# Optimization experiments

Hardware: AMD Instinct MI355X
Metric: run time of the kernel (lower is better)

Reference implementation:

```python
import jax, jax.numpy as jnp
import numpy as np

B, IN_DIM, OUT_DIM, N_KNOTS = 8192, 1024, 1024, 4


def setup_inputs() -> dict:
    key = jax.random.key(0)
    k_feat, k_phase, k_w = jax.random.split(key, 3)
    feats = jax.random.normal(k_feat, (B, IN_DIM), dtype=jnp.float32)
    phase = jax.random.uniform(k_phase, (B, 1), dtype=jnp.float32)  # phase in [0,1)
    x = jnp.concatenate([feats, phase], axis=1)  # [B, IN_DIM+1]
    bound = np.sqrt(6.0 / (OUT_DIM * IN_DIM))
    weight_knots = jax.random.uniform(
        k_w, (N_KNOTS, OUT_DIM, IN_DIM), dtype=jnp.float32, minval=-bound, maxval=bound)
    bias_knots = jnp.zeros((N_KNOTS, OUT_DIM), dtype=jnp.float32)
    return {"x": x, "weight_knots": weight_knots, "bias_knots": bias_knots}


def _cubic(y, mu):
    # Catmull-Rom cubic blend over the 4 gathered knots, y: [B,4,D], mu: [B,1]
    y0, y1, y2, y3 = y[:, 0], y[:, 1], y[:, 2], y[:, 3]
    return ((-0.5 * y0 + 1.5 * y1 - 1.5 * y2 + 0.5 * y3) * mu * mu * mu
            + (y0 - 2.5 * y1 + 2.0 * y2 - 0.5 * y3) * mu * mu
            + (-0.5 * y0 + 0.5 * y2) * mu + y1)


def reference(x, weight_knots, bias_knots):
    K = weight_knots.shape[0]
    phase = x[:, -1]            # [B]
    feats = x[:, :-1]           # [B, IN_DIM]
    pscale = K * phase
    mu = jnp.mod(pscale, 1.0)[:, None]                       # [B, 1]
    i1 = jnp.mod(pscale.astype(jnp.int32), K)
    idx = jnp.stack([jnp.mod(i1 - 1, K), i1,
                     jnp.mod(i1 + 1, K), jnp.mod(i1 + 2, K)], axis=1)  # [B, 4]
    # Exploit linearity: matvec against each knot matrix once, then blend.
    # Mathematically identical to cubic(W0,..,W3) @ feats + cubic(b0,..,b3).
    yk = jnp.einsum('koi,bi->bko', weight_knots, feats)      # [B, K, OUT]
    y4 = jnp.take_along_axis(yk, idx[:, :, None], axis=1)    # [B, 4, OUT]
    b4 = bias_knots[idx]                                     # [B, 4, OUT]
    res = _cubic(y4 + b4, mu)                                # cubic is linear in y
    return jax.nn.elu(res)
```

## Files before the change

kernel.cpp:

```cpp
#include <hip/hip_runtime.h>
#include <math.h>

#define IN_DIM 1024
#define OUT_DIM 1024
#define NROWS 8192
#define XSTRIDE 1025

typedef __attribute__((ext_vector_type(8))) short bf16x8;
typedef __attribute__((ext_vector_type(4))) float f32x4;

static __device__ __forceinline__ unsigned f2bf(float f) {
  union { float f; unsigned u; } v; v.f = f;
  unsigned u = v.u;
  return (u + 0x7fffu + ((u >> 16) & 1u)) >> 16;
}

__global__ __launch_bounds__(256) void prep_kernel(
    const float* __restrict__ x, const float* __restrict__ W,
    unsigned short* __restrict__ Wb, unsigned short* __restrict__ F,
    float* __restrict__ coef)
{
  const int blk = blockIdx.x;
  if (blk < 2048) {
    const int t = blk * 256 + threadIdx.x;
    const int flat = t * 8;
    const int k = flat >> 20;
    const int o = (flat >> 10) & 1023;
    const int i = flat & 1023;
    const float4 fa = *reinterpret_cast<const float4*>(W + flat);
    const float4 fb = *reinterpret_cast<const float4*>(W + flat + 4);
    uint4 pk;
    pk.x = f2bf(fa.x) | (f2bf(fa.y) << 16);
    pk.y = f2bf(fa.z) | (f2bf(fa.w) << 16);
    pk.z = f2bf(fb.x) | (f2bf(fb.y) << 16);
    pk.w = f2bf(fb.z) | (f2bf(fb.w) << 16);
    const int g = (o & 15) | (k << 4) | ((o >> 4) << 6);
    *reinterpret_cast<uint4*>(Wb + (size_t)g * 1024 + i) = pk;
  } else {
    const int b = blk - 2048;
    const float* xr = x + (size_t)b * XSTRIDE;
    const int i = threadIdx.x * 4;
    ushort4 vv;
    vv.x = (unsigned short)f2bf(xr[i]);     vv.y = (unsigned short)f2bf(xr[i + 1]);
    vv.z = (unsigned short)f2bf(xr[i + 2]); vv.w = (unsigned short)f2bf(xr[i + 3]);
    *reinterpret_cast<ushort4*>(F + (size_t)b * 1024 + i) = vv;
    if (threadIdx.x == 0) {
      const float ps = 4.0f * xr[IN_DIM];
      const int ip = (int)ps;
      const int i1 = ip & 3;
      const float mu = ps - (float)ip;
      const float mu2 = mu * mu, mu3 = mu2 * mu;
      const float c0 = -0.5f * mu3 +        mu2 - 0.5f * mu;
      const float c1 =  1.5f * mu3 - 2.5f * mu2 + 1.0f;
      const float c2 = -1.5f * mu3 + 2.0f * mu2 + 0.5f * mu;
      const float c3 =  0.5f * mu3 - 0.5f * mu2;
      const int d0 = (0-i1)&3, d1 = (1-i1)&3, d2 = (2-i1)&3, d3 = (3-i1)&3;
      float4 cv;
      cv.x = d0==0 ? c1 : d0==1 ? c2 : d0==2 ? c3 : c0;
      cv.y = d1==0 ? c1 : d1==1 ? c2 : d1==2 ? c3 : c0;
      cv.z = d2==0 ? c1 : d2==1 ? c2 : d2==2 ? c3 : c0;
      cv.w = d3==0 ? c1 : d3==1 ? c2 : d3==2 ? c3 : c0;
      *reinterpret_cast<float4*>(coef + (size_t)b * 4) = cv;
    }
  }
}

#define BM 128
#define BN 128
#define BK 64

__global__ __launch_bounds__(256, 4) void gemm_kernel(
    const unsigned short* __restrict__ F,
    const unsigned short* __restrict__ Wb,
    const float* __restrict__ coef,
    const float* __restrict__ bias,
    float* __restrict__ out)
{
  __shared__ unsigned short As[BM * BK];
  __shared__ unsigned short Bs[BN * BK];

  const int tid  = threadIdx.x;
  const int wave = tid >> 6;
  const int lane = tid & 63;
  const int row0  = blockIdx.y * BM;
  const int col0g = blockIdx.x * BN;

  const int srow = tid >> 3;
  const int scc  = tid & 7;
  const int sgc  = (scc ^ (srow & 7)) * 8;

  const int wr = (wave >> 1) * 64;
  const int wc = (wave & 1) * 64;
  const int fm = lane & 15;
  const int fq = lane >> 4;

  f32x4 acc[4][4];
  const f32x4 zero = {0.f, 0.f, 0.f, 0.f};
  #pragma unroll
  for (int a = 0; a < 4; a++)
    #pragma unroll
    for (int b = 0; b < 4; b++)
      acc[a][b] = zero;

  const unsigned short* Abase = F  + (size_t)row0  * 1024;
  const unsigned short* Bbase = Wb + (size_t)col0g * 1024;

  for (int kb = 0; kb < 1024; kb += BK) {
    #pragma unroll
    for (int it = 0; it < 4; it++) {
      const int r = srow + it * 32;
      __builtin_amdgcn_global_load_lds(
          (const __attribute__((address_space(1))) void*)(Abase + (size_t)r * 1024 + kb + sgc),
          (__attribute__((address_space(3))) void*)(As + r * BK + scc * 8), 16, 0, 0);
      __builtin_amdgcn_global_load_lds(
          (const __attribute__((address_space(1))) void*)(Bbase + (size_t)r * 1024 + kb + sgc),
          (__attribute__((address_space(3))) void*)(Bs + r * BK + scc * 8), 16, 0, 0);
    }
    __syncthreads();

    #pragma unroll
    for (int kk = 0; kk < BK; kk += 32) {
      bf16x8 af[4], bfr[4];
      #pragma unroll
      for (int mi = 0; mi < 4; mi++) {
        const int r  = wr + mi * 16 + fm;
        const int lc = ((kk >> 3) + fq) ^ (fm & 7);
        af[mi] = *reinterpret_cast<const bf16x8*>(As + r * BK + lc * 8);
      }
      #pragma unroll
      for (int ni = 0; ni < 4; ni++) {
        const int r  = wc + ni * 16 + fm;
        const int lc = ((kk >> 3) + fq) ^ (fm & 7);
        bfr[ni] = *reinterpret_cast<const bf16x8*>(Bs + r * BK + lc * 8);
      }
      #pragma unroll
      for (int mi = 0; mi < 4; mi++)
        #pragma unroll
        for (int ni = 0; ni < 4; ni++)
          acc[mi][ni] = __builtin_amdgcn_mfma_f32_16x16x32_bf16(
              af[mi], bfr[ni], acc[mi][ni], 0, 0, 0);
    }
    __syncthreads();
  }

  const int o = fm + 16 * (2 * blockIdx.x + (wave & 1));
  const float b0 = bias[o];
  const float b1 = bias[OUT_DIM + o];
  const float b2 = bias[2 * OUT_DIM + o];
  const float b3 = bias[3 * OUT_DIM + o];
  #pragma unroll
  for (int mi = 0; mi < 4; mi++) {
    #pragma unroll
    for (int r = 0; r < 4; r++) {
      const int rloc = wr + mi * 16 + (fq << 2) + r;
      const float4 c = *reinterpret_cast<const float4*>(coef + (size_t)(row0 + rloc) * 4);
      float v = c.x * (acc[mi][0][r] + b0)
              + c.y * (acc[mi][1][r] + b1)
              + c.z * (acc[mi][2][r] + b2)
              + c.w * (acc[mi][3][r] + b3);
      const float e = __expf(v) - 1.0f;
      v = (v > 0.0f) ? v : e;
      out[(size_t)(row0 + rloc) * OUT_DIM + o] = v;
    }
  }
}

extern "C" void kernel_launch(void* const* d_in, const int* in_sizes, int n_in,
                              void* d_out, int out_size, void* d_ws, size_t ws_size,
                              hipStream_t stream) {
  const float* x  = (const float*)d_in[0];
  const float* wk = (const float*)d_in[1];
  const float* bk = (const float*)d_in[2];
  float* out = (float*)d_out;

  char* ws = (char*)d_ws;
  unsigned short* Wb = (unsigned short*)ws;
  unsigned short* F  = (unsigned short*)(ws + (8u << 20));
  float* coef        = (float*)(ws + (24u << 20));

  hipLaunchKernelGGL(prep_kernel, dim3(2048 + NROWS), dim3(256), 0, stream,
                     x, wk, Wb, F, coef);
  hipLaunchKernelGGL(gemm_kernel, dim3(4096 / BN, NROWS / BM), dim3(256), 0, stream,
                     F, Wb, coef, bk, out);
}
```

Measured before the change: 160.5 us.

## Use 256x256 tiles with double-buffered LDS and interleaved load/MFMA schedule

Enlarges the GEMM block tile to 256x256 with 8 waves (each 128x64), adds double-buffered LDS, and interleaves the async global-to-LDS loads for the next K tile with MFMA quadrants under explicit barriers, waitcnts and s_setprio. This targets the exposed global load latency and the synchronization stalls of the single-buffered 128x128 loop, and raises arithmetic intensity per LDS byte. The cost is higher register and LDS pressure (128 KB LDS per block, 128 accumulator floats per lane) and fewer blocks, so each CU runs fewer concurrent blocks.

```diff
diff --git a/kernel.cpp b/kernel.cpp
--- a/kernel.cpp
+++ b/kernel.cpp
@@ -65,19 +65,19 @@
   }
 }
 
-#define BM 128
-#define BN 128
+#define BM 256
+#define BN 256
 #define BK 64
 
-__global__ __launch_bounds__(256, 4) void gemm_kernel(
+__global__ __launch_bounds__(512, 2) void gemm_kernel(
     const unsigned short* __restrict__ F,
     const unsigned short* __restrict__ Wb,
     const float* __restrict__ coef,
     const float* __restrict__ bias,
     float* __restrict__ out)
 {
-  __shared__ unsigned short As[BM * BK];
-  __shared__ unsigned short Bs[BN * BK];
+  __shared__ unsigned short As[2][BM * BK];
+  __shared__ unsigned short Bs[2][BN * BK];
 
   const int tid  = threadIdx.x;
   const int wave = tid >> 6;
@@ -89,15 +89,17 @@
   const int scc  = tid & 7;
   const int sgc  = (scc ^ (srow & 7)) * 8;
 
-  const int wr = (wave >> 1) * 64;
-  const int wc = (wave & 1) * 64;
+  const int wr = (wave >> 2) * 128;
+  const int wc = (wave & 3) * 64;
   const int fm = lane & 15;
   const int fq = lane >> 4;
-
-  f32x4 acc[4][4];
+  const int c0 = ((fq    ) ^ (fm & 7)) * 8;
+  const int c1 = ((4 + fq) ^ (fm & 7)) * 8;
+
+  f32x4 acc[8][4];
   const f32x4 zero = {0.f, 0.f, 0.f, 0.f};
   #pragma unroll
-  for (int a = 0; a < 4; a++)
+  for (int a = 0; a < 8; a++)
     #pragma unroll
     for (int b = 0; b < 4; b++)
       acc[a][b] = zero;
@@ -105,53 +107,106 @@
   const unsigned short* Abase = F  + (size_t)row0  * 1024;
   const unsigned short* Bbase = Wb + (size_t)col0g * 1024;
 
-  for (int kb = 0; kb < 1024; kb += BK) {
-    #pragma unroll
-    for (int it = 0; it < 4; it++) {
-      const int r = srow + it * 32;
-      __builtin_amdgcn_global_load_lds(
-          (const __attribute__((address_space(1))) void*)(Abase + (size_t)r * 1024 + kb + sgc),
-          (__attribute__((address_space(3))) void*)(As + r * BK + scc * 8), 16, 0, 0);
-      __builtin_amdgcn_global_load_lds(
-          (const __attribute__((address_space(1))) void*)(Bbase + (size_t)r * 1024 + kb + sgc),
-          (__attribute__((address_space(3))) void*)(Bs + r * BK + scc * 8), 16, 0, 0);
-    }
-    __syncthreads();
-
-    #pragma unroll
-    for (int kk = 0; kk < BK; kk += 32) {
-      bf16x8 af[4], bfr[4];
-      #pragma unroll
-      for (int mi = 0; mi < 4; mi++) {
-        const int r  = wr + mi * 16 + fm;
-        const int lc = ((kk >> 3) + fq) ^ (fm & 7);
-        af[mi] = *reinterpret_cast<const bf16x8*>(As + r * BK + lc * 8);
-      }
-      #pragma unroll
-      for (int ni = 0; ni < 4; ni++) {
-        const int r  = wc + ni * 16 + fm;
-        const int lc = ((kk >> 3) + fq) ^ (fm & 7);
-        bfr[ni] = *reinterpret_cast<const bf16x8*>(Bs + r * BK + lc * 8);
-      }
-      #pragma unroll
-      for (int mi = 0; mi < 4; mi++)
-        #pragma unroll
-        for (int ni = 0; ni < 4; ni++)
-          acc[mi][ni] = __builtin_amdgcn_mfma_f32_16x16x32_bf16(
-              af[mi], bfr[ni], acc[mi][ni], 0, 0, 0);
-    }
-    __syncthreads();
+  bf16x8 areg[4][2];
+  bf16x8 breg[4][2];
+
+#define STAGE(GB, LDSARR, tile, half) do {                                     \
+    _Pragma("unroll")                                                          \
+    for (int j_ = 0; j_ < 2; ++j_) {                                           \
+      const int r_ = ((half) << 7) + (j_ << 6) + srow;                         \
+      __builtin_amdgcn_global_load_lds(                                        \
+        (const __attribute__((address_space(1))) void*)(                       \
+            (GB) + (size_t)r_ * 1024 + ((tile) << 6) + sgc),                   \
+        (__attribute__((address_space(3))) void*)(                             \
+            &LDSARR[(tile) & 1][r_ * BK + scc * 8]),                           \
+        16, 0, 0);                                                             \
+    } } while (0)
+
+#define LDA_QUAD(buf, q)                                                       \
+    _Pragma("unroll")                                                          \
+    for (int mi_ = 0; mi_ < 4; ++mi_) {                                        \
+      const unsigned short* p_ = &As[buf][(wr + (q) * 64 + mi_ * 16 + fm) * BK]; \
+      areg[mi_][0] = *reinterpret_cast<const bf16x8*>(p_ + c0);                \
+      areg[mi_][1] = *reinterpret_cast<const bf16x8*>(p_ + c1);                \
+    }
+
+#define LDB_PAIR(buf, n0)                                                      \
+    _Pragma("unroll")                                                          \
+    for (int ni_ = 0; ni_ < 2; ++ni_) {                                        \
+      const unsigned short* p_ = &Bs[buf][(wc + ((n0) + ni_) * 16 + fm) * BK]; \
+      breg[(n0) + ni_][0] = *reinterpret_cast<const bf16x8*>(p_ + c0);         \
+      breg[(n0) + ni_][1] = *reinterpret_cast<const bf16x8*>(p_ + c1);         \
+    }
+
+#define MFMA_QUAD(q, n0) do {                                                  \
+    __builtin_amdgcn_s_setprio(1);                                             \
+    _Pragma("unroll")                                                          \
+    for (int mi_ = 0; mi_ < 4; ++mi_)                                          \
+      _Pragma("unroll")                                                        \
+      for (int ni_ = 0; ni_ < 2; ++ni_)                                        \
+        _Pragma("unroll")                                                      \
+        for (int s_ = 0; s_ < 2; ++s_)                                         \
+          acc[(q) * 4 + mi_][(n0) + ni_] =                                     \
+              __builtin_amdgcn_mfma_f32_16x16x32_bf16(                         \
+                  areg[mi_][s_], breg[(n0) + ni_][s_],                         \
+                  acc[(q) * 4 + mi_][(n0) + ni_], 0, 0, 0);                    \
+    __builtin_amdgcn_s_setprio(0);                                             \
+  } while (0)
+
+#define BAR __builtin_amdgcn_s_barrier()
+#define LGKM0 do {                                                             \
+    asm volatile("s_waitcnt lgkmcnt(0)" ::: "memory");                         \
+    __builtin_amdgcn_sched_barrier(0);                                         \
+  } while (0)
+
+  STAGE(Abase, As, 0, 0); STAGE(Abase, As, 0, 1);
+  STAGE(Bbase, Bs, 0, 0); STAGE(Bbase, Bs, 0, 1);
+  STAGE(Abase, As, 1, 0); STAGE(Abase, As, 1, 1);
+  STAGE(Bbase, Bs, 1, 0); STAGE(Bbase, Bs, 1, 1);
+  asm volatile("s_waitcnt vmcnt(8)" ::: "memory");
+  BAR;
+
+  #pragma unroll 1
+  for (int i = 0; i < 8; ++i) {
+    const int kt = 2 * i;
+    LDA_QUAD(0, 0);
+    LDB_PAIR(0, 0);
+    if (i >= 1) STAGE(Abase, As, kt + 1, 1);
+    BAR; LGKM0; MFMA_QUAD(0, 0); BAR;
+    LDB_PAIR(0, 2);
+    if (i >= 1) STAGE(Bbase, Bs, kt + 1, 0);
+    BAR; LGKM0; MFMA_QUAD(0, 2); BAR;
+    LDA_QUAD(0, 1);
+    if (i >= 1) STAGE(Bbase, Bs, kt + 1, 1);
+    BAR; LGKM0; MFMA_QUAD(1, 2); BAR;
+    if (i < 7) { STAGE(Abase, As, kt + 2, 0);
+                 asm volatile("s_waitcnt vmcnt(2)" ::: "memory"); }
+    else       { asm volatile("s_waitcnt vmcnt(0)" ::: "memory"); }
+    BAR; __builtin_amdgcn_sched_barrier(0); MFMA_QUAD(1, 0); BAR;
+    LDA_QUAD(1, 0);
+    LDB_PAIR(1, 0);
+    if (i < 7) STAGE(Abase, As, kt + 2, 1);
+    BAR; LGKM0; MFMA_QUAD(0, 0); BAR;
+    LDB_PAIR(1, 2);
+    if (i < 7) STAGE(Bbase, Bs, kt + 2, 0);
+    BAR; LGKM0; MFMA_QUAD(0, 2); BAR;
+    LDA_QUAD(1, 1);
+    if (i < 7) STAGE(Bbase, Bs, kt + 2, 1);
+    BAR; LGKM0; MFMA_QUAD(1, 2); BAR;
+    if (i < 7) { STAGE(Abase, As, kt + 3, 0);
+                 asm volatile("s_waitcnt vmcnt(2)" ::: "memory"); }
+    BAR; __builtin_amdgcn_sched_barrier(0); MFMA_QUAD(1, 0); BAR;
   }
 
-  const int o = fm + 16 * (2 * blockIdx.x + (wave & 1));
+  const int o = fm + 16 * ((col0g + wc) >> 6);
   const float b0 = bias[o];
   const float b1 = bias[OUT_DIM + o];
   const float b2 = bias[2 * OUT_DIM + o];
   const float b3 = bias[3 * OUT_DIM + o];
   #pragma unroll
-  for (int mi = 0; mi < 4; mi++) {
+  for (int mi = 0; mi < 8; ++mi) {
     #pragma unroll
-    for (int r = 0; r < 4; r++) {
+    for (int r = 0; r < 4; ++r) {
       const int rloc = wr + mi * 16 + (fq << 2) + r;
       const float4 c = *reinterpret_cast<const float4*>(coef + (size_t)(row0 + rloc) * 4);
       float v = c.x * (acc[mi][0][r] + b0)
@@ -163,6 +218,12 @@
       out[(size_t)(row0 + rloc) * OUT_DIM + o] = v;
     }
   }
+#undef STAGE
+#undef LDA_QUAD
+#undef LDB_PAIR
+#undef MFMA_QUAD
+#undef BAR
+#undef LGKM0
 }
 
 extern "C" void kernel_launch(void* const* d_in, const int* in_sizes, int n_in,
@@ -180,6 +241,6 @@
 
   hipLaunchKernelGGL(prep_kernel, dim3(2048 + NROWS), dim3(256), 0, stream,
                      x, wk, Wb, F, coef);
-  hipLaunchKernelGGL(gemm_kernel, dim3(4096 / BN, NROWS / BM), dim3(256), 0, stream,
+  hipLaunchKernelGGL(gemm_kernel, dim3(4096 / BN, NROWS / BM), dim3(512), 0, stream,
                      F, Wb, coef, bk, out);
 }
```

New measurement: 163.4 us. Within noise of the previous version (+1.8%).
